# Kernel optimization log

Hardware: AMD Instinct MI355X
Metric: run time of the kernel (lower is better)

Reference implementation:

```python
import jax, jax.numpy as jnp
import numpy as np

N, IN_DIM, L, K, D = 131072, 128, 16, 8, 50
ENC_H, DEC_H, HEAD_H, DF = 64, 16, 64, 1.0


def setup_inputs() -> dict:
    key = jax.random.key(0)
    ks = jax.random.split(key, 20)
    s = lambda k, shape, fan: jax.random.normal(k, shape, jnp.float32) * (1.0 / np.sqrt(fan))
    return {
        "x": jax.random.normal(ks[0], (N, IN_DIM), jnp.float32),
        # encoder: in -> 64 -> 64 -> L
        "We1": s(ks[1], (IN_DIM, ENC_H), IN_DIM), "be1": jnp.zeros((ENC_H,), jnp.float32),
        "We2": s(ks[2], (ENC_H, ENC_H), ENC_H),   "be2": jnp.zeros((ENC_H,), jnp.float32),
        "We3": s(ks[3], (ENC_H, L), ENC_H),       "be3": jnp.zeros((L,), jnp.float32),
        # decoder: L -> 16 -> in
        "Wd1": s(ks[4], (L, DEC_H), L),           "bd1": jnp.zeros((DEC_H,), jnp.float32),
        "Wd2": s(ks[5], (DEC_H, IN_DIM), DEC_H),  "bd2": jnp.zeros((IN_DIM,), jnp.float32),
        # K per-cluster survival heads: (L+in) -> 64 -> num_durations
        "Wh1": s(ks[6], (K, L + IN_DIM, HEAD_H), L + IN_DIM), "bh1": jnp.zeros((K, HEAD_H), jnp.float32),
        "Wh2": s(ks[7], (K, HEAD_H, D), HEAD_H),              "bh2": jnp.zeros((K, D), jnp.float32),
        # cluster centers buffer
        "centers": jax.random.normal(ks[8], (K, L), jnp.float32) * 0.05,
    }


def _student_t_sim(z, centers, df):
    # z: [N, L], centers: [K, L] -> q: [N, K]
    dist2 = jnp.sum((z[:, None, :] - centers[None, :, :]) ** 2, axis=-1)
    logits = -0.5 * (df + 1.0) * jnp.log1p(dist2 / df)
    return jax.nn.softmax(logits, axis=1)


def reference(x, We1, be1, We2, be2, We3, be3, Wd1, bd1, Wd2, bd2,
              Wh1, bh1, Wh2, bh2, centers):
    relu = jax.nn.relu
    # encoder (eval mode: dropout off, non-variational)
    e = relu(x @ We1 + be1)
    e = relu(e @ We2 + be2)
    z = e @ We3 + be3                      # [N, L]
    q = _student_t_sim(z, centers, DF)     # [N, K]
    h = jnp.concatenate([z, x], axis=1)    # [N, L+in]
    # cluster-argmax routing to per-cluster heads: compute all K, select winner
    cluster_idx = jnp.argmax(q, axis=1)    # [N]
    h1 = relu(jnp.einsum("nf,kfh->nkh", h, Wh1) + bh1[None])   # [N, K, H]
    lg = jnp.einsum("nkh,khd->nkd", h1, Wh2) + bh2[None]       # [N, K, D]
    surv_logits = jnp.take_along_axis(lg, cluster_idx[:, None, None], axis=1)[:, 0]  # [N, D]
    # decoder + reconstruction loss per sample
    d = relu(z @ Wd1 + bd1)
    x_hat = d @ Wd2 + bd2                  # [N, in]
    rec_ps = jnp.mean((x_hat - x) ** 2, axis=1)
    kld = jnp.zeros((x.shape[0],), x.dtype)
    return z, q, surv_logits, x_hat, rec_ps, kld
```

## Files before the change

### kernel.cpp

```cpp
#include <hip/hip_runtime.h>

#define NS 131072
#define KC 8
typedef unsigned long long u64;

#define LD4(P) (*reinterpret_cast<const float4*>(&sm[(P)]))
#define LD2(P) (*reinterpret_cast<const float2*>(&sm[(P)]))
#define ST4(P) (*reinterpret_cast<float4*>(&sm[(P)]))
#define ST2(P) (*reinterpret_cast<float2*>(&sm[(P)]))
#define GL4(P) (*reinterpret_cast<const float4*>(&(P)))

#define FMA8(ACCR, AV, W0, W1) do { \
  ACCR[0]=fmaf((AV),(W0).x,ACCR[0]); ACCR[1]=fmaf((AV),(W0).y,ACCR[1]); \
  ACCR[2]=fmaf((AV),(W0).z,ACCR[2]); ACCR[3]=fmaf((AV),(W0).w,ACCR[3]); \
  ACCR[4]=fmaf((AV),(W1).x,ACCR[4]); ACCR[5]=fmaf((AV),(W1).y,ACCR[5]); \
  ACCR[6]=fmaf((AV),(W1).z,ACCR[6]); ACCR[7]=fmaf((AV),(W1).w,ACCR[7]); } while(0)

#define K4(ACC, ABASE, ASTR, AK, BBASE, BSTR, JOFF, BK) do { \
  const float4 b00=LD4((BBASE)+((BK)*4+0)*(BSTR)+(JOFF)), b01=LD4((BBASE)+((BK)*4+0)*(BSTR)+(JOFF)+4); \
  const float4 b10=LD4((BBASE)+((BK)*4+1)*(BSTR)+(JOFF)), b11=LD4((BBASE)+((BK)*4+1)*(BSTR)+(JOFF)+4); \
  const float4 b20=LD4((BBASE)+((BK)*4+2)*(BSTR)+(JOFF)), b21=LD4((BBASE)+((BK)*4+2)*(BSTR)+(JOFF)+4); \
  const float4 b30=LD4((BBASE)+((BK)*4+3)*(BSTR)+(JOFF)), b31=LD4((BBASE)+((BK)*4+3)*(BSTR)+(JOFF)+4); \
  _Pragma("unroll") \
  for (int m_ = 0; m_ < 8; ++m_) { \
    const float4 av = LD4((ABASE)+(st+32*m_)*(ASTR)+(AK)*4); \
    FMA8(ACC[m_], av.x, b00, b01); FMA8(ACC[m_], av.y, b10, b11); \
    FMA8(ACC[m_], av.z, b20, b21); FMA8(ACC[m_], av.w, b30, b31); } \
} while(0)

#define INIT88(ACC, BPTR, OFF) do { \
  const float4 u_ = *reinterpret_cast<const float4*>(&(BPTR)[(OFF)]); \
  const float4 v_ = *reinterpret_cast<const float4*>(&(BPTR)[(OFF)+4]); \
  _Pragma("unroll") for (int m_ = 0; m_ < 8; ++m_) { \
    ACC[m_][0]=u_.x; ACC[m_][1]=u_.y; ACC[m_][2]=u_.z; ACC[m_][3]=u_.w; \
    ACC[m_][4]=v_.x; ACC[m_][5]=v_.y; ACC[m_][6]=v_.z; ACC[m_][7]=v_.w; } \
} while(0)

#define RELU88(ACC) do { _Pragma("unroll") for (int m_=0;m_<8;++m_) \
  { _Pragma("unroll") for (int j_=0;j_<8;++j_) ACC[m_][j_]=fmaxf(ACC[m_][j_],0.f); } } while(0)

#define WRITE_E(ACC) do { _Pragma("unroll") for (int m_=0;m_<8;++m_){ \
  const int r_ = st + 32*m_; \
  ST4(AR + r_*68 + job)     = make_float4(ACC[m_][0],ACC[m_][1],ACC[m_][2],ACC[m_][3]); \
  ST4(AR + r_*68 + job + 4) = make_float4(ACC[m_][4],ACC[m_][5],ACC[m_][6],ACC[m_][7]); } } while(0)

#define STAGE_X() do { \
  ST4(AR + (xr0      )*20 + xc) = rx0; \
  ST4(AR + (xr0 +  64)*20 + xc) = rx1; \
  ST4(AR + (xr0 + 128)*20 + xc) = rx2; \
  ST4(AR + (xr0 + 192)*20 + xc) = rx3; } while(0)

#define AR  0
#define WB  17408
#define WD1 18496
#define SMW 18752

__global__ __launch_bounds__(256, 1) void k_enc(
    const float* __restrict__ x,
    const float* __restrict__ We1, const float* __restrict__ be1,
    const float* __restrict__ We2, const float* __restrict__ be2,
    const float* __restrict__ We3, const float* __restrict__ be3,
    const float* __restrict__ Wd1, const float* __restrict__ bd1,
    const float* __restrict__ Wd2, const float* __restrict__ bd2,
    const float* __restrict__ centers,
    float* __restrict__ out_z, float* __restrict__ out_q,
    float* __restrict__ xhat, float* __restrict__ rec, float* __restrict__ kld,
    int* __restrict__ cidx, int* __restrict__ counts)
{
    __shared__ float sm[SMW];
    const int t  = threadIdx.x;
    const int ot = t & 7, st = t >> 3;
    const int job = ot * 8;
    const int s0 = blockIdx.x * 256;
    const int xr0 = t >> 2, xc = (t & 3) * 4;
    const int wr  = t >> 4, wc = (t & 15) * 4;

    {
        float acc1[8][8];
        INIT88(acc1, be1, job);
        float4 rx0 = GL4(x[(size_t)(s0+xr0      )*128 + xc]);
        float4 rx1 = GL4(x[(size_t)(s0+xr0 +  64)*128 + xc]);
        float4 rx2 = GL4(x[(size_t)(s0+xr0 + 128)*128 + xc]);
        float4 rx3 = GL4(x[(size_t)(s0+xr0 + 192)*128 + xc]);
        float4 rw  = GL4(We1[(size_t)wr*64 + wc]);
        #pragma unroll 1
        for (int c = 0; c < 8; ++c) {
            __syncthreads();
            STAGE_X();
            ST4(WB + wr*68 + wc) = rw;
            __syncthreads();
            if (c < 7) {
                rx0 = GL4(x[(size_t)(s0+xr0      )*128 + (c+1)*16 + xc]);
                rx1 = GL4(x[(size_t)(s0+xr0 +  64)*128 + (c+1)*16 + xc]);
                rx2 = GL4(x[(size_t)(s0+xr0 + 128)*128 + (c+1)*16 + xc]);
                rx3 = GL4(x[(size_t)(s0+xr0 + 192)*128 + (c+1)*16 + xc]);
                rw  = GL4(We1[(size_t)((c+1)*16 + wr)*64 + wc]);
            }
            #pragma unroll
            for (int kc = 0; kc < 4; ++kc) K4(acc1, AR, 20, kc, WB, 68, job, kc);
        }
        __syncthreads();
        RELU88(acc1);
        WRITE_E(acc1);
    }

    {
        float acc2[8][8];
        INIT88(acc2, be2, job);
        float4 rw = GL4(We2[(size_t)wr*64 + wc]);
        #pragma unroll 1
        for (int c = 0; c < 4; ++c) {
            __syncthreads();
            ST4(WB + wr*68 + wc) = rw;
            __syncthreads();
            if (c < 3) rw = GL4(We2[(size_t)((c+1)*16 + wr)*64 + wc]);
            #pragma unroll
            for (int kc = 0; kc < 4; ++kc) K4(acc2, AR, 68, c*4 + kc, WB, 68, job, kc);
        }
        __syncthreads();
        RELU88(acc2);
        WRITE_E(acc2);
    }
    {   const int row = t >> 2, c4 = (t & 3) * 4;
        ST4(WB + row*16 + c4) = GL4(We3[(size_t)row*16 + c4]); }
    if (t < 64) ST4(WD1 + (t >> 2)*16 + (t & 3)*4) =
        GL4(Wd1[(t >> 2)*16 + (t & 3)*4]);
    __syncthreads();

    float zac[8][2];
    {   const float2 b3 = *reinterpret_cast<const float2*>(&be3[ot*2]);
        #pragma unroll
        for (int m = 0; m < 8; ++m) { zac[m][0] = b3.x; zac[m][1] = b3.y; } }
    #pragma unroll 2
    for (int kc = 0; kc < 16; ++kc) {
        const float2 w0 = LD2(WB + (kc*4+0)*16 + ot*2);
        const float2 w1 = LD2(WB + (kc*4+1)*16 + ot*2);
        const float2 w2 = LD2(WB + (kc*4+2)*16 + ot*2);
        const float2 w3 = LD2(WB + (kc*4+3)*16 + ot*2);
        #pragma unroll
        for (int m = 0; m < 8; ++m) {
            const float4 av = LD4(AR + (st + 32*m)*68 + kc*4);
            float sa = zac[m][0], sb = zac[m][1];
            sa = fmaf(av.x, w0.x, sa); sb = fmaf(av.x, w0.y, sb);
            sa = fmaf(av.y, w1.x, sa); sb = fmaf(av.y, w1.y, sb);
            sa = fmaf(av.z, w2.x, sa); sb = fmaf(av.z, w2.y, sb);
            sa = fmaf(av.w, w3.x, sa); sb = fmaf(av.w, w3.y, sb);
            zac[m][0] = sa; zac[m][1] = sb;
        }
    }
    #pragma unroll
    for (int m = 0; m < 8; ++m)
        *reinterpret_cast<float2*>(&out_z[(size_t)(s0 + st + 32*m)*16 + ot*2]) =
            make_float2(zac[m][0], zac[m][1]);
    __syncthreads();
    #pragma unroll
    for (int m = 0; m < 8; ++m)
        ST2(AR + (st + 32*m)*20 + ot*2) = make_float2(zac[m][0], zac[m][1]);
    {
        ST4(WB + wr*68 + wc) = GL4(Wd2[(size_t)wr*128 + wc]); }
    __syncthreads();

    {
        const float4 z0 = LD4(AR + t*20 + 0), z1 = LD4(AR + t*20 + 4);
        const float4 z2 = LD4(AR + t*20 + 8), z3 = LD4(AR + t*20 + 12);
        const float zz[16] = {z0.x,z0.y,z0.z,z0.w, z1.x,z1.y,z1.z,z1.w,
                              z2.x,z2.y,z2.z,z2.w, z3.x,z3.y,z3.z,z3.w};
        float d2[KC];
        #pragma unroll
        for (int k = 0; k < KC; ++k) {
            float acc = 0.f;
            #pragma unroll
            for (int l = 0; l < 16; ++l) {
                const float dl = zz[l] - centers[k*16 + l];
                acc = fmaf(dl, dl, acc);
            }
            d2[k] = acc;
        }
        float lgt[KC], ex[KC];
        float mm = -1e30f;
        #pragma unroll
        for (int k = 0; k < KC; ++k) { lgt[k] = -log1pf(d2[k]); mm = fmaxf(mm, lgt[k]); }
        float ssum = 0.f;
        #pragma unroll
        for (int k = 0; k < KC; ++k) { ex[k] = expf(lgt[k] - mm); ssum += ex[k]; }
        const float inv = 1.f / ssum;
        float4* oq = reinterpret_cast<float4*>(&out_q[(size_t)(s0 + t)*8]);
        oq[0] = make_float4(ex[0]*inv, ex[1]*inv, ex[2]*inv, ex[3]*inv);
        oq[1] = make_float4(ex[4]*inv, ex[5]*inv, ex[6]*inv, ex[7]*inv);
        int ci = 0; float best = d2[0];
        #pragma unroll
        for (int k = 1; k < KC; ++k) if (d2[k] < best) { best = d2[k]; ci = k; }
        cidx[s0 + t] = ci;
        #pragma unroll
        for (int k = 0; k < KC; ++k) {
            const u64 mk = __ballot(ci == k);
            if ((t & 63) == 0 && mk) atomicAdd(&counts[k], (int)__popcll(mk));
        }
        kld[s0 + t] = 0.f;
    }

    {
        float dac[8][2];
        const float2 bb = *reinterpret_cast<const float2*>(&bd1[ot*2]);
        const float2 u0 = LD2(WD1 + 0*16 + ot*2),  u1 = LD2(WD1 + 1*16 + ot*2);
        const float2 u2 = LD2(WD1 + 2*16 + ot*2),  u3 = LD2(WD1 + 3*16 + ot*2);
        const float2 u4 = LD2(WD1 + 4*16 + ot*2),  u5 = LD2(WD1 + 5*16 + ot*2);
        const float2 u6 = LD2(WD1 + 6*16 + ot*2),  u7 = LD2(WD1 + 7*16 + ot*2);
        const float2 u8 = LD2(WD1 + 8*16 + ot*2),  u9 = LD2(WD1 + 9*16 + ot*2);
        const float2 uA = LD2(WD1 + 10*16 + ot*2), uB = LD2(WD1 + 11*16 + ot*2);
        const float2 uC = LD2(WD1 + 12*16 + ot*2), uD = LD2(WD1 + 13*16 + ot*2);
        const float2 uE = LD2(WD1 + 14*16 + ot*2), uF = LD2(WD1 + 15*16 + ot*2);
        #pragma unroll
        for (int m = 0; m < 8; ++m) {
            const int r = st + 32*m;
            const float4 a0 = LD4(AR + r*20 + 0), a1 = LD4(AR + r*20 + 4);
            const float4 a2 = LD4(AR + r*20 + 8), a3 = LD4(AR + r*20 + 12);
            float sa = bb.x, sb = bb.y;
            sa=fmaf(a0.x,u0.x,sa); sb=fmaf(a0.x,u0.y,sb);
            sa=fmaf(a0.y,u1.x,sa); sb=fmaf(a0.y,u1.y,sb);
            sa=fmaf(a0.z,u2.x,sa); sb=fmaf(a0.z,u2.y,sb);
            sa=fmaf(a0.w,u3.x,sa); sb=fmaf(a0.w,u3.y,sb);
            sa=fmaf(a1.x,u4.x,sa); sb=fmaf(a1.x,u4.y,sb);
            sa=fmaf(a1.y,u5.x,sa); sb=fmaf(a1.y,u5.y,sb);
            sa=fmaf(a1.z,u6.x,sa); sb=fmaf(a1.z,u6.y,sb);
            sa=fmaf(a1.w,u7.x,sa); sb=fmaf(a1.w,u7.y,sb);
            sa=fmaf(a2.x,u8.x,sa); sb=fmaf(a2.x,u8.y,sb);
            sa=fmaf(a2.y,u9.x,sa); sb=fmaf(a2.y,u9.y,sb);
            sa=fmaf(a2.z,uA.x,sa); sb=fmaf(a2.z,uA.y,sb);
            sa=fmaf(a2.w,uB.x,sa); sb=fmaf(a2.w,uB.y,sb);
            sa=fmaf(a3.x,uC.x,sa); sb=fmaf(a3.x,uC.y,sb);
            sa=fmaf(a3.y,uD.x,sa); sb=fmaf(a3.y,uD.y,sb);
            sa=fmaf(a3.z,uE.x,sa); sb=fmaf(a3.z,uE.y,sb);
            sa=fmaf(a3.w,uF.x,sa); sb=fmaf(a3.w,uF.y,sb);
            dac[m][0] = fmaxf(sa, 0.f); dac[m][1] = fmaxf(sb, 0.f);
        }
        __syncthreads();
        #pragma unroll
        for (int m = 0; m < 8; ++m)
            ST2(AR + (st + 32*m)*20 + ot*2) = make_float2(dac[m][0], dac[m][1]);
    }
    __syncthreads();

    float rp[8] = {0.f,0.f,0.f,0.f,0.f,0.f,0.f,0.f};
    float4 rw2 = GL4(Wd2[(size_t)wr*128 + 64 + wc]);
    {
        float accx[8][8];
        INIT88(accx, bd2, job);
        #pragma unroll
        for (int kc = 0; kc < 4; ++kc) K4(accx, AR, 20, kc, WB, 68, job, kc);
        #pragma unroll
        for (int m = 0; m < 8; ++m) {
            const int r = st + 32*m;
            const float4 xa = GL4(x[(size_t)(s0+r)*128 + job]);
            const float4 xb = GL4(x[(size_t)(s0+r)*128 + job + 4]);
            float df;
            df=accx[m][0]-xa.x; rp[m]=fmaf(df,df,rp[m]);
            df=accx[m][1]-xa.y; rp[m]=fmaf(df,df,rp[m]);
            df=accx[m][2]-xa.z; rp[m]=fmaf(df,df,rp[m]);
            df=accx[m][3]-xa.w; rp[m]=fmaf(df,df,rp[m]);
            df=accx[m][4]-xb.x; rp[m]=fmaf(df,df,rp[m]);
            df=accx[m][5]-xb.y; rp[m]=fmaf(df,df,rp[m]);
            df=accx[m][6]-xb.z; rp[m]=fmaf(df,df,rp[m]);
            df=accx[m][7]-xb.w; rp[m]=fmaf(df,df,rp[m]);
            float4* o = reinterpret_cast<float4*>(&xhat[(size_t)(s0+r)*128 + job]);
            o[0] = make_float4(accx[m][0],accx[m][1],accx[m][2],accx[m][3]);
            o[1] = make_float4(accx[m][4],accx[m][5],accx[m][6],accx[m][7]);
        }
    }
    __syncthreads();
    ST4(WB + wr*68 + wc) = rw2;
    __syncthreads();
    {
        float accx[8][8];
        INIT88(accx, bd2, 64 + job);
        #pragma unroll
        for (int kc = 0; kc < 4; ++kc) K4(accx, AR, 20, kc, WB, 68, job, kc);
        #pragma unroll
        for (int m = 0; m < 8; ++m) {
            const int r = st + 32*m;
            const float4 xa = GL4(x[(size_t)(s0+r)*128 + 64 + job]);
            const float4 xb = GL4(x[(size_t)(s0+r)*128 + 64 + job + 4]);
            float df;
            df=accx[m][0]-xa.x; rp[m]=fmaf(df,df,rp[m]);
            df=accx[m][1]-xa.y; rp[m]=fmaf(df,df,rp[m]);
            df=accx[m][2]-xa.z; rp[m]=fmaf(df,df,rp[m]);
            df=accx[m][3]-xa.w; rp[m]=fmaf(df,df,rp[m]);
            df=accx[m][4]-xb.x; rp[m]=fmaf(df,df,rp[m]);
            df=accx[m][5]-xb.y; rp[m]=fmaf(df,df,rp[m]);
            df=accx[m][6]-xb.z; rp[m]=fmaf(df,df,rp[m]);
            df=accx[m][7]-xb.w; rp[m]=fmaf(df,df,rp[m]);
            float4* o = reinterpret_cast<float4*>(&xhat[(size_t)(s0+r)*128 + 64 + job]);
            o[0] = make_float4(accx[m][0],accx[m][1],accx[m][2],accx[m][3]);
            o[1] = make_float4(accx[m][4],accx[m][5],accx[m][6],accx[m][7]);
        }
    }
    #pragma unroll
    for (int m = 0; m < 8; ++m) {
        float v = rp[m];
        v += __shfl_xor(v, 1); v += __shfl_xor(v, 2); v += __shfl_xor(v, 4);
        if (ot == 0) rec[s0 + st + 32*m] = v * (1.f/128.f);
    }
}

__global__ void k_scan(const int* __restrict__ counts,
                       int* __restrict__ bases, int* __restrict__ cursors)
{
    if (threadIdx.x == 0) {
        int acc = 0;
        for (int k = 0; k < KC; ++k) { bases[k] = acc; cursors[k] = acc; acc += counts[k]; }
    }
}

__global__ __launch_bounds__(256) void k_scatter(
    const int* __restrict__ cidx, int* __restrict__ cursors, int* __restrict__ seg)
{
    const int s = blockIdx.x * 256 + threadIdx.x;
    const int lane = threadIdx.x & 63;
    const int ci = cidx[s];
    #pragma unroll
    for (int k = 0; k < KC; ++k) {
        const u64 mk = __ballot(ci == k);
        if (ci == k) {
            const int leader = __ffsll(mk) - 1;
            int base = 0;
            if (lane == leader) base = atomicAdd(&cursors[k], (int)__popcll(mk));
            base = __shfl(base, leader, 64);
            seg[base + (int)__popcll(mk & (((u64)1 << lane) - 1))] = s;
        }
    }
}

#define SMH 18496

__global__ __launch_bounds__(256, 1) void k_heads(
    const float* __restrict__ x, const float* __restrict__ zread,
    const float* __restrict__ Wh1, const float* __restrict__ bh1,
    const float* __restrict__ Wh2, const float* __restrict__ bh2,
    const int* __restrict__ counts, const int* __restrict__ bases,
    const int* __restrict__ seg,
    float* __restrict__ surv)
{
    __shared__ float sm[SMH];
    __shared__ int idxs[256];
    const int t  = threadIdx.x;
    const int ot = t & 7, st = t >> 3;
    const int job = ot * 8;
    const int xr0 = t >> 2, xc = (t & 3) * 4;
    const int wr  = t >> 4, wc = (t & 15) * 4;

    int kk = -1, chunk = 0, pref = 0;
    #pragma unroll
    for (int q = 0; q < KC; ++q) {
        const int ck = (counts[q] + 255) >> 8;
        if (kk < 0) {
            if ((int)blockIdx.x < pref + ck) { kk = q; chunk = (int)blockIdx.x - pref; }
            pref += ck;
        }
    }
    if (kk < 0) return;
    kk    = __builtin_amdgcn_readfirstlane(kk);
    chunk = __builtin_amdgcn_readfirstlane(chunk);
    const int cnt  = __builtin_amdgcn_readfirstlane(counts[kk]);
    const int base = __builtin_amdgcn_readfirstlane(bases[kk]);

    {   const int i = chunk*256 + t;
        idxs[t] = seg[base + ((i < cnt) ? i : (cnt - 1))]; }
    __syncthreads();
    const int i0 = idxs[xr0], i1 = idxs[xr0+64], i2 = idxs[xr0+128], i3 = idxs[xr0+192];

    {
        float acc1[8][8];
        INIT88(acc1, bh1, (size_t)kk*64 + job);
        {   const int zc = (t & 3) * 4;
            ST4(AR + (xr0      )*20 + zc) = GL4(zread[(size_t)i0*16 + zc]);
            ST4(AR + (xr0 +  64)*20 + zc) = GL4(zread[(size_t)i1*16 + zc]);
            ST4(AR + (xr0 + 128)*20 + zc) = GL4(zread[(size_t)i2*16 + zc]);
            ST4(AR + (xr0 + 192)*20 + zc) = GL4(zread[(size_t)i3*16 + zc]);
            ST4(WB + wr*68 + wc) = GL4(Wh1[((size_t)kk*144 + wr)*64 + wc]); }
        __syncthreads();
        float4 rx0 = GL4(x[(size_t)i0*128 + xc]);
        float4 rx1 = GL4(x[(size_t)i1*128 + xc]);
        float4 rx2 = GL4(x[(size_t)i2*128 + xc]);
        float4 rx3 = GL4(x[(size_t)i3*128 + xc]);
        float4 rw  = GL4(Wh1[((size_t)kk*144 + 16 + wr)*64 + wc]);
        #pragma unroll
        for (int kc = 0; kc < 4; ++kc) K4(acc1, AR, 20, kc, WB, 68, job, kc);
        #pragma unroll 1
        for (int c = 0; c < 8; ++c) {
            __syncthreads();
            STAGE_X();
            ST4(WB + wr*68 + wc) = rw;
            __syncthreads();
            if (c < 7) {
                rx0 = GL4(x[(size_t)i0*128 + (c+1)*16 + xc]);
                rx1 = GL4(x[(size_t)i1*128 + (c+1)*16 + xc]);
                rx2 = GL4(x[(size_t)i2*128 + (c+1)*16 + xc]);
                rx3 = GL4(x[(size_t)i3*128 + (c+1)*16 + xc]);
                rw  = GL4(Wh1[((size_t)kk*144 + 16 + (c+1)*16 + wr)*64 + wc]);
            }
            #pragma unroll
            for (int kc = 0; kc < 4; ++kc) K4(acc1, AR, 20, kc, WB, 68, job, kc);
        }
        __syncthreads();
        RELU88(acc1);
        WRITE_E(acc1);
    }

    float acc2[8][8];
    {   float bz[8];
        #pragma unroll
        for (int j = 0; j < 8; ++j) {
            const int col = job + j;
            bz[j] = (col < 50) ? bh2[(size_t)kk*50 + col] : 0.f;
        }
        #pragma unroll
        for (int m = 0; m < 8; ++m) {
            #pragma unroll
            for (int j = 0; j < 8; ++j) acc2[m][j] = bz[j];
        } }
    float4 rv;
    {   const int gk = wr;
        rv.x = (wc+0 < 50) ? Wh2[((size_t)kk*64 + gk)*50 + wc+0] : 0.f;
        rv.y = (wc+1 < 50) ? Wh2[((size_t)kk*64 + gk)*50 + wc+1] : 0.f;
        rv.z = (wc+2 < 50) ? Wh2[((size_t)kk*64 + gk)*50 + wc+2] : 0.f;
        rv.w = (wc+3 < 50) ? Wh2[((size_t)kk*64 + gk)*50 + wc+3] : 0.f; }
    #pragma unroll 1
    for (int c = 0; c < 4; ++c) {
        __syncthreads();
        ST4(WB + wr*68 + wc) = rv;
        __syncthreads();
        if (c < 3) {
            const int gk = (c+1)*16 + wr;
            rv.x = (wc+0 < 50) ? Wh2[((size_t)kk*64 + gk)*50 + wc+0] : 0.f;
            rv.y = (wc+1 < 50) ? Wh2[((size_t)kk*64 + gk)*50 + wc+1] : 0.f;
            rv.z = (wc+2 < 50) ? Wh2[((size_t)kk*64 + gk)*50 + wc+2] : 0.f;
            rv.w = (wc+3 < 50) ? Wh2[((size_t)kk*64 + gk)*50 + wc+3] : 0.f;
        }
        #pragma unroll
        for (int kc = 0; kc < 4; ++kc) K4(acc2, AR, 68, c*4 + kc, WB, 68, job, kc);
    }

    #pragma unroll
    for (int m = 0; m < 8; ++m) {
        const int r = st + 32*m;
        if (chunk*256 + r < cnt) {
            float* so = &surv[(size_t)idxs[r]*50 + job];
            if (ot < 6) {
                *reinterpret_cast<float2*>(&so[0]) = make_float2(acc2[m][0], acc2[m][1]);
                *reinterpret_cast<float2*>(&so[2]) = make_float2(acc2[m][2], acc2[m][3]);
                *reinterpret_cast<float2*>(&so[4]) = make_float2(acc2[m][4], acc2[m][5]);
                *reinterpret_cast<float2*>(&so[6]) = make_float2(acc2[m][6], acc2[m][7]);
            } else if (ot == 6) {
                *reinterpret_cast<float2*>(&so[0]) = make_float2(acc2[m][0], acc2[m][1]);
            }
        }
    }
}

extern "C" void kernel_launch(void* const* d_in, const int* in_sizes, int n_in,
                              void* d_out, int out_size, void* d_ws, size_t ws_size,
                              hipStream_t stream)
{
    const float* x   = (const float*)d_in[0];
    const float* We1 = (const float*)d_in[1];
    const float* be1 = (const float*)d_in[2];
    const float* We2 = (const float*)d_in[3];
    const float* be2 = (const float*)d_in[4];
    const float* We3 = (const float*)d_in[5];
    const float* be3 = (const float*)d_in[6];
    const float* Wd1 = (const float*)d_in[7];
    const float* bd1 = (const float*)d_in[8];
    const float* Wd2 = (const float*)d_in[9];
    const float* bd2 = (const float*)d_in[10];
    const float* Wh1 = (const float*)d_in[11];
    const float* bh1 = (const float*)d_in[12];
    const float* Wh2 = (const float*)d_in[13];
    const float* bh2 = (const float*)d_in[14];
    const float* cen = (const float*)d_in[15];
    float* out = (float*)d_out;

    float* out_z  = out;
    float* out_q  = out + (size_t)NS * 16;
    float* out_sv = out + (size_t)NS * 24;
    float* out_xh = out + (size_t)NS * 74;
    float* out_rc = out + (size_t)NS * 202;
    float* out_kl = out + (size_t)NS * 203;

    int* cidx    = (int*)d_ws;
    int* counts  = cidx + NS;
    int* bases   = counts + KC;
    int* cursors = bases + KC;
    int* seg     = cursors + KC;

    hipMemsetAsync(counts, 0, KC * sizeof(int), stream);

    k_enc<<<dim3(NS / 256), dim3(256), 0, stream>>>(
        x, We1, be1, We2, be2, We3, be3, Wd1, bd1, Wd2, bd2, cen,
        out_z, out_q, out_xh, out_rc, out_kl, cidx, counts);

    k_scan<<<dim3(1), dim3(64), 0, stream>>>(counts, bases, cursors);

    k_scatter<<<dim3(NS / 256), dim3(256), 0, stream>>>(cidx, cursors, seg);

    k_heads<<<dim3(NS / 256 + KC), dim3(256), 0, stream>>>(
        x, out_z, Wh1, bh1, Wh2, bh2, counts, bases, seg, out_sv);
}
```

Baseline: 501.6 us.

## Halve rows per block and per-thread tile to raise occupancy in encoder and heads

Both k_enc and k_heads now process 128 samples per block instead of 256, with each thread owning an 8x4 output tile instead of 8x8, 16 threads across columns, and a smaller shared-memory footprint. Launch bounds go from 1 to 2 blocks per SIMD/CU and the grids double. The aim is more resident waves to hide global and LDS latency, at the cost of less register-level reuse of each loaded weight and activation and more block-level overhead and barriers per sample. The 16-column z and decoder stages now use one output column per thread, and only half the threads run the softmax/argmax section.

```diff
diff --git a/kernel.cpp b/kernel.cpp
--- a/kernel.cpp
+++ b/kernel.cpp
@@ -5,57 +5,47 @@
 typedef unsigned long long u64;
 
 #define LD4(P) (*reinterpret_cast<const float4*>(&sm[(P)]))
-#define LD2(P) (*reinterpret_cast<const float2*>(&sm[(P)]))
 #define ST4(P) (*reinterpret_cast<float4*>(&sm[(P)]))
-#define ST2(P) (*reinterpret_cast<float2*>(&sm[(P)]))
 #define GL4(P) (*reinterpret_cast<const float4*>(&(P)))
 
-#define FMA8(ACCR, AV, W0, W1) do { \
-  ACCR[0]=fmaf((AV),(W0).x,ACCR[0]); ACCR[1]=fmaf((AV),(W0).y,ACCR[1]); \
-  ACCR[2]=fmaf((AV),(W0).z,ACCR[2]); ACCR[3]=fmaf((AV),(W0).w,ACCR[3]); \
-  ACCR[4]=fmaf((AV),(W1).x,ACCR[4]); ACCR[5]=fmaf((AV),(W1).y,ACCR[5]); \
-  ACCR[6]=fmaf((AV),(W1).z,ACCR[6]); ACCR[7]=fmaf((AV),(W1).w,ACCR[7]); } while(0)
+#define FMA4(ACCR, AV, B) do { \
+  ACCR[0]=fmaf((AV),(B).x,ACCR[0]); ACCR[1]=fmaf((AV),(B).y,ACCR[1]); \
+  ACCR[2]=fmaf((AV),(B).z,ACCR[2]); ACCR[3]=fmaf((AV),(B).w,ACCR[3]); } while(0)
 
 #define K4(ACC, ABASE, ASTR, AK, BBASE, BSTR, JOFF, BK) do { \
-  const float4 b00=LD4((BBASE)+((BK)*4+0)*(BSTR)+(JOFF)), b01=LD4((BBASE)+((BK)*4+0)*(BSTR)+(JOFF)+4); \
-  const float4 b10=LD4((BBASE)+((BK)*4+1)*(BSTR)+(JOFF)), b11=LD4((BBASE)+((BK)*4+1)*(BSTR)+(JOFF)+4); \
-  const float4 b20=LD4((BBASE)+((BK)*4+2)*(BSTR)+(JOFF)), b21=LD4((BBASE)+((BK)*4+2)*(BSTR)+(JOFF)+4); \
-  const float4 b30=LD4((BBASE)+((BK)*4+3)*(BSTR)+(JOFF)), b31=LD4((BBASE)+((BK)*4+3)*(BSTR)+(JOFF)+4); \
+  const float4 b0=LD4((BBASE)+((BK)*4+0)*(BSTR)+(JOFF)); \
+  const float4 b1=LD4((BBASE)+((BK)*4+1)*(BSTR)+(JOFF)); \
+  const float4 b2=LD4((BBASE)+((BK)*4+2)*(BSTR)+(JOFF)); \
+  const float4 b3=LD4((BBASE)+((BK)*4+3)*(BSTR)+(JOFF)); \
   _Pragma("unroll") \
   for (int m_ = 0; m_ < 8; ++m_) { \
-    const float4 av = LD4((ABASE)+(st+32*m_)*(ASTR)+(AK)*4); \
-    FMA8(ACC[m_], av.x, b00, b01); FMA8(ACC[m_], av.y, b10, b11); \
-    FMA8(ACC[m_], av.z, b20, b21); FMA8(ACC[m_], av.w, b30, b31); } \
+    const float4 av = LD4((ABASE)+(st+16*m_)*(ASTR)+(AK)*4); \
+    FMA4(ACC[m_], av.x, b0); FMA4(ACC[m_], av.y, b1); \
+    FMA4(ACC[m_], av.z, b2); FMA4(ACC[m_], av.w, b3); } \
 } while(0)
 
-#define INIT88(ACC, BPTR, OFF) do { \
+#define INIT84(ACC, BPTR, OFF) do { \
   const float4 u_ = *reinterpret_cast<const float4*>(&(BPTR)[(OFF)]); \
-  const float4 v_ = *reinterpret_cast<const float4*>(&(BPTR)[(OFF)+4]); \
-  _Pragma("unroll") for (int m_ = 0; m_ < 8; ++m_) { \
-    ACC[m_][0]=u_.x; ACC[m_][1]=u_.y; ACC[m_][2]=u_.z; ACC[m_][3]=u_.w; \
-    ACC[m_][4]=v_.x; ACC[m_][5]=v_.y; ACC[m_][6]=v_.z; ACC[m_][7]=v_.w; } \
-} while(0)
-
-#define RELU88(ACC) do { _Pragma("unroll") for (int m_=0;m_<8;++m_) \
-  { _Pragma("unroll") for (int j_=0;j_<8;++j_) ACC[m_][j_]=fmaxf(ACC[m_][j_],0.f); } } while(0)
+  _Pragma("unroll") for (int m_=0;m_<8;++m_){ \
+    ACC[m_][0]=u_.x; ACC[m_][1]=u_.y; ACC[m_][2]=u_.z; ACC[m_][3]=u_.w; } } while(0)
+
+#define RELU84(ACC) do { _Pragma("unroll") for (int m_=0;m_<8;++m_) \
+  { _Pragma("unroll") for (int j_=0;j_<4;++j_) ACC[m_][j_]=fmaxf(ACC[m_][j_],0.f); } } while(0)
 
 #define WRITE_E(ACC) do { _Pragma("unroll") for (int m_=0;m_<8;++m_){ \
-  const int r_ = st + 32*m_; \
-  ST4(AR + r_*68 + job)     = make_float4(ACC[m_][0],ACC[m_][1],ACC[m_][2],ACC[m_][3]); \
-  ST4(AR + r_*68 + job + 4) = make_float4(ACC[m_][4],ACC[m_][5],ACC[m_][6],ACC[m_][7]); } } while(0)
+  ST4(AR + (st+16*m_)*68 + job) = \
+    make_float4(ACC[m_][0],ACC[m_][1],ACC[m_][2],ACC[m_][3]); } } while(0)
 
 #define STAGE_X() do { \
-  ST4(AR + (xr0      )*20 + xc) = rx0; \
-  ST4(AR + (xr0 +  64)*20 + xc) = rx1; \
-  ST4(AR + (xr0 + 128)*20 + xc) = rx2; \
-  ST4(AR + (xr0 + 192)*20 + xc) = rx3; } while(0)
-
-#define AR  0
-#define WB  17408
-#define WD1 18496
-#define SMW 18752
-
-__global__ __launch_bounds__(256, 1) void k_enc(
+  ST4(AR + xr0*20 + xcc)     = rx0; \
+  ST4(AR + xr0*20 + xcc + 4) = rx1; } while(0)
+
+#define AR   0
+#define WD1i 2560
+#define WB   8704
+#define SMW  9792
+
+__global__ __launch_bounds__(256, 2) void k_enc(
     const float* __restrict__ x,
     const float* __restrict__ We1, const float* __restrict__ be1,
     const float* __restrict__ We2, const float* __restrict__ be2,
@@ -69,19 +59,17 @@
 {
     __shared__ float sm[SMW];
     const int t  = threadIdx.x;
-    const int ot = t & 7, st = t >> 3;
-    const int job = ot * 8;
-    const int s0 = blockIdx.x * 256;
-    const int xr0 = t >> 2, xc = (t & 3) * 4;
-    const int wr  = t >> 4, wc = (t & 15) * 4;
-
-    {
-        float acc1[8][8];
-        INIT88(acc1, be1, job);
-        float4 rx0 = GL4(x[(size_t)(s0+xr0      )*128 + xc]);
-        float4 rx1 = GL4(x[(size_t)(s0+xr0 +  64)*128 + xc]);
-        float4 rx2 = GL4(x[(size_t)(s0+xr0 + 128)*128 + xc]);
-        float4 rx3 = GL4(x[(size_t)(s0+xr0 + 192)*128 + xc]);
+    const int ot = t & 15, st = t >> 4;
+    const int job = ot * 4;
+    const int s0 = blockIdx.x * 128;
+    const int xr0 = t >> 1, xcc = (t & 1) * 8;
+    const int wr  = t >> 4, wc  = (t & 15) * 4;
+
+    {
+        float acc1[8][4];
+        INIT84(acc1, be1, job);
+        float4 rx0 = GL4(x[(size_t)(s0+xr0)*128 + xcc]);
+        float4 rx1 = GL4(x[(size_t)(s0+xr0)*128 + xcc + 4]);
         float4 rw  = GL4(We1[(size_t)wr*64 + wc]);
         #pragma unroll 1
         for (int c = 0; c < 8; ++c) {
@@ -90,23 +78,21 @@
             ST4(WB + wr*68 + wc) = rw;
             __syncthreads();
             if (c < 7) {
-                rx0 = GL4(x[(size_t)(s0+xr0      )*128 + (c+1)*16 + xc]);
-                rx1 = GL4(x[(size_t)(s0+xr0 +  64)*128 + (c+1)*16 + xc]);
-                rx2 = GL4(x[(size_t)(s0+xr0 + 128)*128 + (c+1)*16 + xc]);
-                rx3 = GL4(x[(size_t)(s0+xr0 + 192)*128 + (c+1)*16 + xc]);
+                rx0 = GL4(x[(size_t)(s0+xr0)*128 + (c+1)*16 + xcc]);
+                rx1 = GL4(x[(size_t)(s0+xr0)*128 + (c+1)*16 + xcc + 4]);
                 rw  = GL4(We1[(size_t)((c+1)*16 + wr)*64 + wc]);
             }
             #pragma unroll
             for (int kc = 0; kc < 4; ++kc) K4(acc1, AR, 20, kc, WB, 68, job, kc);
         }
         __syncthreads();
-        RELU88(acc1);
+        RELU84(acc1);
         WRITE_E(acc1);
     }
 
     {
-        float acc2[8][8];
-        INIT88(acc2, be2, job);
+        float acc2[8][4];
+        INIT84(acc2, be2, job);
         float4 rw = GL4(We2[(size_t)wr*64 + wc]);
         #pragma unroll 1
         for (int c = 0; c < 4; ++c) {
@@ -118,49 +104,44 @@
             for (int kc = 0; kc < 4; ++kc) K4(acc2, AR, 68, c*4 + kc, WB, 68, job, kc);
         }
         __syncthreads();
-        RELU88(acc2);
+        RELU84(acc2);
         WRITE_E(acc2);
     }
     {   const int row = t >> 2, c4 = (t & 3) * 4;
         ST4(WB + row*16 + c4) = GL4(We3[(size_t)row*16 + c4]); }
-    if (t < 64) ST4(WD1 + (t >> 2)*16 + (t & 3)*4) =
-        GL4(Wd1[(t >> 2)*16 + (t & 3)*4]);
-    __syncthreads();
-
-    float zac[8][2];
-    {   const float2 b3 = *reinterpret_cast<const float2*>(&be3[ot*2]);
-        #pragma unroll
-        for (int m = 0; m < 8; ++m) { zac[m][0] = b3.x; zac[m][1] = b3.y; } }
+    __syncthreads();
+
+    float zac[8];
+    {   const float b3v = be3[ot];
+        #pragma unroll
+        for (int m = 0; m < 8; ++m) zac[m] = b3v; }
     #pragma unroll 2
     for (int kc = 0; kc < 16; ++kc) {
-        const float2 w0 = LD2(WB + (kc*4+0)*16 + ot*2);
-        const float2 w1 = LD2(WB + (kc*4+1)*16 + ot*2);
-        const float2 w2 = LD2(WB + (kc*4+2)*16 + ot*2);
-        const float2 w3 = LD2(WB + (kc*4+3)*16 + ot*2);
+        const float w0 = sm[WB + (kc*4+0)*16 + ot];
+        const float w1 = sm[WB + (kc*4+1)*16 + ot];
+        const float w2 = sm[WB + (kc*4+2)*16 + ot];
+        const float w3 = sm[WB + (kc*4+3)*16 + ot];
         #pragma unroll
         for (int m = 0; m < 8; ++m) {
-            const float4 av = LD4(AR + (st + 32*m)*68 + kc*4);
-            float sa = zac[m][0], sb = zac[m][1];
-            sa = fmaf(av.x, w0.x, sa); sb = fmaf(av.x, w0.y, sb);
-            sa = fmaf(av.y, w1.x, sa); sb = fmaf(av.y, w1.y, sb);
-            sa = fmaf(av.z, w2.x, sa); sb = fmaf(av.z, w2.y, sb);
-            sa = fmaf(av.w, w3.x, sa); sb = fmaf(av.w, w3.y, sb);
-            zac[m][0] = sa; zac[m][1] = sb;
+            const float4 av = LD4(AR + (st + 16*m)*68 + kc*4);
+            float s = zac[m];
+            s = fmaf(av.x, w0, s); s = fmaf(av.y, w1, s);
+            s = fmaf(av.z, w2, s); s = fmaf(av.w, w3, s);
+            zac[m] = s;
         }
     }
     #pragma unroll
     for (int m = 0; m < 8; ++m)
-        *reinterpret_cast<float2*>(&out_z[(size_t)(s0 + st + 32*m)*16 + ot*2]) =
-            make_float2(zac[m][0], zac[m][1]);
-    __syncthreads();
-    #pragma unroll
-    for (int m = 0; m < 8; ++m)
-        ST2(AR + (st + 32*m)*20 + ot*2) = make_float2(zac[m][0], zac[m][1]);
-    {
-        ST4(WB + wr*68 + wc) = GL4(Wd2[(size_t)wr*128 + wc]); }
-    __syncthreads();
-
-    {
+        out_z[(size_t)(s0 + st + 16*m)*16 + ot] = zac[m];
+    __syncthreads();
+    #pragma unroll
+    for (int m = 0; m < 8; ++m) sm[AR + (st + 16*m)*20 + ot] = zac[m];
+    ST4(WB + wr*68 + wc) = GL4(Wd2[(size_t)wr*128 + wc]);
+    if (t < 64) ST4(WD1i + (t >> 2)*16 + (t & 3)*4) =
+        GL4(Wd1[(t >> 2)*16 + (t & 3)*4]);
+    __syncthreads();
+
+    if (t < 128) {
         const float4 z0 = LD4(AR + t*20 + 0), z1 = LD4(AR + t*20 + 4);
         const float4 z2 = LD4(AR + t*20 + 8), z3 = LD4(AR + t*20 + 12);
         const float zz[16] = {z0.x,z0.y,z0.z,z0.w, z1.x,z1.y,z1.z,z1.w,
@@ -200,105 +181,76 @@
     }
 
     {
-        float dac[8][2];
-        const float2 bb = *reinterpret_cast<const float2*>(&bd1[ot*2]);
-        const float2 u0 = LD2(WD1 + 0*16 + ot*2),  u1 = LD2(WD1 + 1*16 + ot*2);
-        const float2 u2 = LD2(WD1 + 2*16 + ot*2),  u3 = LD2(WD1 + 3*16 + ot*2);
-        const float2 u4 = LD2(WD1 + 4*16 + ot*2),  u5 = LD2(WD1 + 5*16 + ot*2);
-        const float2 u6 = LD2(WD1 + 6*16 + ot*2),  u7 = LD2(WD1 + 7*16 + ot*2);
-        const float2 u8 = LD2(WD1 + 8*16 + ot*2),  u9 = LD2(WD1 + 9*16 + ot*2);
-        const float2 uA = LD2(WD1 + 10*16 + ot*2), uB = LD2(WD1 + 11*16 + ot*2);
-        const float2 uC = LD2(WD1 + 12*16 + ot*2), uD = LD2(WD1 + 13*16 + ot*2);
-        const float2 uE = LD2(WD1 + 14*16 + ot*2), uF = LD2(WD1 + 15*16 + ot*2);
+        float w[16];
+        #pragma unroll
+        for (int k = 0; k < 16; ++k) w[k] = sm[WD1i + k*16 + ot];
+        const float bb = bd1[ot];
+        float dac[8];
         #pragma unroll
         for (int m = 0; m < 8; ++m) {
-            const int r = st + 32*m;
-            const float4 a0 = LD4(AR + r*20 + 0), a1 = LD4(AR + r*20 + 4);
-            const float4 a2 = LD4(AR + r*20 + 8), a3 = LD4(AR + r*20 + 12);
-            float sa = bb.x, sb = bb.y;
-            sa=fmaf(a0.x,u0.x,sa); sb=fmaf(a0.x,u0.y,sb);
-            sa=fmaf(a0.y,u1.x,sa); sb=fmaf(a0.y,u1.y,sb);
-            sa=fmaf(a0.z,u2.x,sa); sb=fmaf(a0.z,u2.y,sb);
-            sa=fmaf(a0.w,u3.x,sa); sb=fmaf(a0.w,u3.y,sb);
-            sa=fmaf(a1.x,u4.x,sa); sb=fmaf(a1.x,u4.y,sb);
-            sa=fmaf(a1.y,u5.x,sa); sb=fmaf(a1.y,u5.y,sb);
-            sa=fmaf(a1.z,u6.x,sa); sb=fmaf(a1.z,u6.y,sb);
-            sa=fmaf(a1.w,u7.x,sa); sb=fmaf(a1.w,u7.y,sb);
-            sa=fmaf(a2.x,u8.x,sa); sb=fmaf(a2.x,u8.y,sb);
-            sa=fmaf(a2.y,u9.x,sa); sb=fmaf(a2.y,u9.y,sb);
-            sa=fmaf(a2.z,uA.x,sa); sb=fmaf(a2.z,uA.y,sb);
-            sa=fmaf(a2.w,uB.x,sa); sb=fmaf(a2.w,uB.y,sb);
-            sa=fmaf(a3.x,uC.x,sa); sb=fmaf(a3.x,uC.y,sb);
-            sa=fmaf(a3.y,uD.x,sa); sb=fmaf(a3.y,uD.y,sb);
-            sa=fmaf(a3.z,uE.x,sa); sb=fmaf(a3.z,uE.y,sb);
-            sa=fmaf(a3.w,uF.x,sa); sb=fmaf(a3.w,uF.y,sb);
-            dac[m][0] = fmaxf(sa, 0.f); dac[m][1] = fmaxf(sb, 0.f);
-        }
-        __syncthreads();
-        #pragma unroll
-        for (int m = 0; m < 8; ++m)
-            ST2(AR + (st + 32*m)*20 + ot*2) = make_float2(dac[m][0], dac[m][1]);
+            const int r = st + 16*m;
+            float s = bb;
+            #pragma unroll
+            for (int kc = 0; kc < 4; ++kc) {
+                const float4 av = LD4(AR + r*20 + kc*4);
+                s = fmaf(av.x, w[kc*4+0], s); s = fmaf(av.y, w[kc*4+1], s);
+                s = fmaf(av.z, w[kc*4+2], s); s = fmaf(av.w, w[kc*4+3], s);
+            }
+            dac[m] = fmaxf(s, 0.f);
+        }
+        __syncthreads();
+        #pragma unroll
+        for (int m = 0; m < 8; ++m) sm[AR + (st + 16*m)*20 + ot] = dac[m];
     }
     __syncthreads();
 
     float rp[8] = {0.f,0.f,0.f,0.f,0.f,0.f,0.f,0.f};
     float4 rw2 = GL4(Wd2[(size_t)wr*128 + 64 + wc]);
     {
-        float accx[8][8];
-        INIT88(accx, bd2, job);
+        float accx[8][4];
+        INIT84(accx, bd2, job);
         #pragma unroll
         for (int kc = 0; kc < 4; ++kc) K4(accx, AR, 20, kc, WB, 68, job, kc);
         #pragma unroll
         for (int m = 0; m < 8; ++m) {
-            const int r = st + 32*m;
+            const int r = st + 16*m;
             const float4 xa = GL4(x[(size_t)(s0+r)*128 + job]);
-            const float4 xb = GL4(x[(size_t)(s0+r)*128 + job + 4]);
             float df;
             df=accx[m][0]-xa.x; rp[m]=fmaf(df,df,rp[m]);
             df=accx[m][1]-xa.y; rp[m]=fmaf(df,df,rp[m]);
             df=accx[m][2]-xa.z; rp[m]=fmaf(df,df,rp[m]);
             df=accx[m][3]-xa.w; rp[m]=fmaf(df,df,rp[m]);
-            df=accx[m][4]-xb.x; rp[m]=fmaf(df,df,rp[m]);
-            df=accx[m][5]-xb.y; rp[m]=fmaf(df,df,rp[m]);
-            df=accx[m][6]-xb.z; rp[m]=fmaf(df,df,rp[m]);
-            df=accx[m][7]-xb.w; rp[m]=fmaf(df,df,rp[m]);
-            float4* o = reinterpret_cast<float4*>(&xhat[(size_t)(s0+r)*128 + job]);
-            o[0] = make_float4(accx[m][0],accx[m][1],accx[m][2],accx[m][3]);
-            o[1] = make_float4(accx[m][4],accx[m][5],accx[m][6],accx[m][7]);
+            *reinterpret_cast<float4*>(&xhat[(size_t)(s0+r)*128 + job]) =
+                make_float4(accx[m][0],accx[m][1],accx[m][2],accx[m][3]);
         }
     }
     __syncthreads();
     ST4(WB + wr*68 + wc) = rw2;
     __syncthreads();
     {
-        float accx[8][8];
-        INIT88(accx, bd2, 64 + job);
+        float accx[8][4];
+        INIT84(accx, bd2, 64 + job);
         #pragma unroll
         for (int kc = 0; kc < 4; ++kc) K4(accx, AR, 20, kc, WB, 68, job, kc);
         #pragma unroll
         for (int m = 0; m < 8; ++m) {
-            const int r = st + 32*m;
+            const int r = st + 16*m;
             const float4 xa = GL4(x[(size_t)(s0+r)*128 + 64 + job]);
-            const float4 xb = GL4(x[(size_t)(s0+r)*128 + 64 + job + 4]);
             float df;
             df=accx[m][0]-xa.x; rp[m]=fmaf(df,df,rp[m]);
             df=accx[m][1]-xa.y; rp[m]=fmaf(df,df,rp[m]);
             df=accx[m][2]-xa.z; rp[m]=fmaf(df,df,rp[m]);
             df=accx[m][3]-xa.w; rp[m]=fmaf(df,df,rp[m]);
-            df=accx[m][4]-xb.x; rp[m]=fmaf(df,df,rp[m]);
-            df=accx[m][5]-xb.y; rp[m]=fmaf(df,df,rp[m]);
-            df=accx[m][6]-xb.z; rp[m]=fmaf(df,df,rp[m]);
-            df=accx[m][7]-xb.w; rp[m]=fmaf(df,df,rp[m]);
-            float4* o = reinterpret_cast<float4*>(&xhat[(size_t)(s0+r)*128 + 64 + job]);
-            o[0] = make_float4(accx[m][0],accx[m][1],accx[m][2],accx[m][3]);
-            o[1] = make_float4(accx[m][4],accx[m][5],accx[m][6],accx[m][7]);
+            *reinterpret_cast<float4*>(&xhat[(size_t)(s0+r)*128 + 64 + job]) =
+                make_float4(accx[m][0],accx[m][1],accx[m][2],accx[m][3]);
         }
     }
     #pragma unroll
     for (int m = 0; m < 8; ++m) {
         float v = rp[m];
-        v += __shfl_xor(v, 1); v += __shfl_xor(v, 2); v += __shfl_xor(v, 4);
-        if (ot == 0) rec[s0 + st + 32*m] = v * (1.f/128.f);
+        v += __shfl_xor(v, 1); v += __shfl_xor(v, 2);
+        v += __shfl_xor(v, 4); v += __shfl_xor(v, 8);
+        if (ot == 0) rec[s0 + st + 16*m] = v * (1.f/128.f);
     }
 }
 
@@ -330,9 +282,7 @@
     }
 }
 
-#define SMH 18496
-
-__global__ __launch_bounds__(256, 1) void k_heads(
+__global__ __launch_bounds__(256, 2) void k_heads(
     const float* __restrict__ x, const float* __restrict__ zread,
     const float* __restrict__ Wh1, const float* __restrict__ bh1,
     const float* __restrict__ Wh2, const float* __restrict__ bh2,
@@ -340,18 +290,18 @@
     const int* __restrict__ seg,
     float* __restrict__ surv)
 {
-    __shared__ float sm[SMH];
-    __shared__ int idxs[256];
+    __shared__ float sm[SMW];
+    __shared__ int idxs[128];
     const int t  = threadIdx.x;
-    const int ot = t & 7, st = t >> 3;
-    const int job = ot * 8;
-    const int xr0 = t >> 2, xc = (t & 3) * 4;
-    const int wr  = t >> 4, wc = (t & 15) * 4;
+    const int ot = t & 15, st = t >> 4;
+    const int job = ot * 4;
+    const int xr0 = t >> 1, xcc = (t & 1) * 8;
+    const int wr  = t >> 4, wc  = (t & 15) * 4;
 
     int kk = -1, chunk = 0, pref = 0;
     #pragma unroll
     for (int q = 0; q < KC; ++q) {
-        const int ck = (counts[q] + 255) >> 8;
+        const int ck = (counts[q] + 127) >> 7;
         if (kk < 0) {
             if ((int)blockIdx.x < pref + ck) { kk = q; chunk = (int)blockIdx.x - pref; }
             pref += ck;
@@ -363,25 +313,23 @@
     const int cnt  = __builtin_amdgcn_readfirstlane(counts[kk]);
     const int base = __builtin_amdgcn_readfirstlane(bases[kk]);
 
-    {   const int i = chunk*256 + t;
-        idxs[t] = seg[base + ((i < cnt) ? i : (cnt - 1))]; }
-    __syncthreads();
-    const int i0 = idxs[xr0], i1 = idxs[xr0+64], i2 = idxs[xr0+128], i3 = idxs[xr0+192];
-
-    {
-        float acc1[8][8];
-        INIT88(acc1, bh1, (size_t)kk*64 + job);
-        {   const int zc = (t & 3) * 4;
-            ST4(AR + (xr0      )*20 + zc) = GL4(zread[(size_t)i0*16 + zc]);
-            ST4(AR + (xr0 +  64)*20 + zc) = GL4(zread[(size_t)i1*16 + zc]);
-            ST4(AR + (xr0 + 128)*20 + zc) = GL4(zread[(size_t)i2*16 + zc]);
-            ST4(AR + (xr0 + 192)*20 + zc) = GL4(zread[(size_t)i3*16 + zc]);
+    if (t < 128) {
+        const int i = chunk*128 + t;
+        idxs[t] = seg[base + ((i < cnt) ? i : (cnt - 1))];
+    }
+    __syncthreads();
+    const int irow = idxs[xr0];
+
+    {
+        float acc1[8][4];
+        INIT84(acc1, bh1, (size_t)kk*64 + job);
+        {
+            ST4(AR + xr0*20 + xcc)     = GL4(zread[(size_t)irow*16 + xcc]);
+            ST4(AR + xr0*20 + xcc + 4) = GL4(zread[(size_t)irow*16 + xcc + 4]);
             ST4(WB + wr*68 + wc) = GL4(Wh1[((size_t)kk*144 + wr)*64 + wc]); }
         __syncthreads();
-        float4 rx0 = GL4(x[(size_t)i0*128 + xc]);
-        float4 rx1 = GL4(x[(size_t)i1*128 + xc]);
-        float4 rx2 = GL4(x[(size_t)i2*128 + xc]);
-        float4 rx3 = GL4(x[(size_t)i3*128 + xc]);
+        float4 rx0 = GL4(x[(size_t)irow*128 + xcc]);
+        float4 rx1 = GL4(x[(size_t)irow*128 + xcc + 4]);
         float4 rw  = GL4(Wh1[((size_t)kk*144 + 16 + wr)*64 + wc]);
         #pragma unroll
         for (int kc = 0; kc < 4; ++kc) K4(acc1, AR, 20, kc, WB, 68, job, kc);
@@ -392,31 +340,28 @@
             ST4(WB + wr*68 + wc) = rw;
             __syncthreads();
             if (c < 7) {
-                rx0 = GL4(x[(size_t)i0*128 + (c+1)*16 + xc]);
-                rx1 = GL4(x[(size_t)i1*128 + (c+1)*16 + xc]);
-                rx2 = GL4(x[(size_t)i2*128 + (c+1)*16 + xc]);
-                rx3 = GL4(x[(size_t)i3*128 + (c+1)*16 + xc]);
+                rx0 = GL4(x[(size_t)irow*128 + (c+1)*16 + xcc]);
+                rx1 = GL4(x[(size_t)irow*128 + (c+1)*16 + xcc + 4]);
                 rw  = GL4(Wh1[((size_t)kk*144 + 16 + (c+1)*16 + wr)*64 + wc]);
             }
             #pragma unroll
             for (int kc = 0; kc < 4; ++kc) K4(acc1, AR, 20, kc, WB, 68, job, kc);
         }
         __syncthreads();
-        RELU88(acc1);
+        RELU84(acc1);
         WRITE_E(acc1);
     }
 
-    float acc2[8][8];
-    {   float bz[8];
-        #pragma unroll
-        for (int j = 0; j < 8; ++j) {
-            const int col = job + j;
-            bz[j] = (col < 50) ? bh2[(size_t)kk*50 + col] : 0.f;
-        }
+    float acc2[8][4];
+    {   float4 bz;
+        bz.x = (job+0 < 50) ? bh2[(size_t)kk*50 + job+0] : 0.f;
+        bz.y = (job+1 < 50) ? bh2[(size_t)kk*50 + job+1] : 0.f;
+        bz.z = (job+2 < 50) ? bh2[(size_t)kk*50 + job+2] : 0.f;
+        bz.w = (job+3 < 50) ? bh2[(size_t)kk*50 + job+3] : 0.f;
         #pragma unroll
         for (int m = 0; m < 8; ++m) {
-            #pragma unroll
-            for (int j = 0; j < 8; ++j) acc2[m][j] = bz[j];
+            acc2[m][0] = bz.x; acc2[m][1] = bz.y;
+            acc2[m][2] = bz.z; acc2[m][3] = bz.w;
         } }
     float4 rv;
     {   const int gk = wr;
@@ -442,15 +387,13 @@
 
     #pragma unroll
     for (int m = 0; m < 8; ++m) {
-        const int r = st + 32*m;
-        if (chunk*256 + r < cnt) {
+        const int r = st + 16*m;
+        if (chunk*128 + r < cnt) {
             float* so = &surv[(size_t)idxs[r]*50 + job];
-            if (ot < 6) {
+            if (ot < 12) {
                 *reinterpret_cast<float2*>(&so[0]) = make_float2(acc2[m][0], acc2[m][1]);
                 *reinterpret_cast<float2*>(&so[2]) = make_float2(acc2[m][2], acc2[m][3]);
-                *reinterpret_cast<float2*>(&so[4]) = make_float2(acc2[m][4], acc2[m][5]);
-                *reinterpret_cast<float2*>(&so[6]) = make_float2(acc2[m][6], acc2[m][7]);
-            } else if (ot == 6) {
+            } else if (ot == 12) {
                 *reinterpret_cast<float2*>(&so[0]) = make_float2(acc2[m][0], acc2[m][1]);
             }
         }
@@ -494,7 +437,7 @@
 
     hipMemsetAsync(counts, 0, KC * sizeof(int), stream);
 
-    k_enc<<<dim3(NS / 256), dim3(256), 0, stream>>>(
+    k_enc<<<dim3(NS / 128), dim3(256), 0, stream>>>(
         x, We1, be1, We2, be2, We3, be3, Wd1, bd1, Wd2, bd2, cen,
         out_z, out_q, out_xh, out_rc, out_kl, cidx, counts);
 
@@ -502,6 +445,6 @@
 
     k_scatter<<<dim3(NS / 256), dim3(256), 0, stream>>>(cidx, cursors, seg);
 
-    k_heads<<<dim3(NS / 256 + KC), dim3(256), 0, stream>>>(
+    k_heads<<<dim3(NS / 128 + KC), dim3(256), 0, stream>>>(
         x, out_z, Wh1, bh1, Wh2, bh2, counts, bases, seg, out_sv);
 }
```

Measured after the change: 447.0 us. -10.9%, faster.
